# Optimization experiments

Hardware: AMD Instinct MI355X
Metric: run time of the kernel (lower is better)

The kernel has to match this reference:

```python
import jax, jax.numpy as jnp
import numpy as np

B, L, D, K = 32, 128, 400, 40
RTOL, ATOL = 1e-4, 1e-6


def setup_inputs() -> dict:
    key = jax.random.key(0)
    ks = jax.random.split(key, 9)
    s = 0.3                      # input scale keeps exp(energy) in fp32 range
    u = 1.0 / np.sqrt(D)         # param scale
    input_h = jax.random.normal(ks[0], (B, L, D), jnp.float32) * s
    input_c = jax.random.normal(ks[1], (B, L, D), jnp.float32) * s
    W_d = jax.random.normal(ks[2], (K, D), jnp.float32) * u
    W_e = jax.random.normal(ks[3], (K, D), jnp.float32) * u
    U = jax.random.normal(ks[4], (K, D, D), jnp.float32) * u
    b = jax.random.normal(ks[5], (K,), jnp.float32) * 0.1
    heads = jax.random.randint(ks[6], (B, L), 0, L)
    pos = jnp.arange(L)[None, :]
    heads = jnp.where(heads == pos, (heads + 1) % L, heads)  # no self-loops (diag is -inf)
    arc_tags = jax.random.randint(ks[7], (B, L), 0, K)
    lengths = jax.random.randint(ks[8], (B,), L // 2, L + 1)
    mask = (jnp.arange(L)[None, :] < lengths[:, None]).astype(jnp.float32)
    return {"input_h": input_h, "input_c": input_c, "W_d": W_d, "W_e": W_e,
            "U": U, "b": b, "mask": mask, "heads": heads,
            "arc_tags": arc_tags, "lengths": lengths}


def reference(input_h, input_c, W_d, W_e, U, b, mask, heads, arc_tags, lengths):
    Bsz, Ln, _ = input_h.shape
    # --- BiAAttention: energy[b,k,head,child] ---
    bil = jnp.einsum('bhd,kde,bce->bkhc', input_h, U, input_c)
    sd = jnp.einsum('kd,bhd->bkh', W_d, input_h)[:, :, :, None]   # head bias
    se = jnp.einsum('kd,bcd->bkc', W_e, input_c)[:, :, None, :]   # child bias
    energy = bil + sd + se + b[None, :, None, None]
    energy = energy * mask[:, None, :, None] * mask[:, None, None, :]
    eye = jnp.eye(Ln, dtype=energy.dtype)
    energy = energy + jnp.where(eye > 0, -jnp.inf, 0.0)           # no self-arcs
    # --- Matrix-Tree partition function ---
    A = jnp.exp(energy) * mask[:, None, :, None] * mask[:, None, None, :]
    A = A.sum(axis=1)                                             # [B,L,L] over labels
    Dg = A.sum(axis=1) * (1.0 + RTOL) + ATOL                      # column (in-degree) sums
    Lap = eye * Dg[:, None, :] - A                                # Laplacian
    Sub = Lap[:, 1:, 1:]                                          # drop root row/col
    valid = jnp.arange(Ln - 1)[None, :] < (lengths - 1)[:, None]
    vm = valid[:, :, None] & valid[:, None, :]
    Sub = jnp.where(vm, Sub, jnp.eye(Ln - 1, dtype=Sub.dtype))    # identity-pad = logdet of [1:len,1:len]
    z = jnp.linalg.slogdet(Sub)[1]                                # [B]
    # --- gold-tree energy ---
    bi = jnp.arange(Bsz)[:, None]
    pos = jnp.arange(Ln)[None, :]
    te = energy[bi, arc_tags, heads, pos]                         # [B,L]
    tgt = te[:, 1:].sum(axis=1)
    return z - tgt
```

## Files before the change

### kernel.cpp

```cpp
#include <hip/hip_runtime.h>
#include <hip/hip_bf16.h>

#define BB 32
#define LL 128
#define DD 400
#define KK 40
#define EE 416
#define SDN 50
#define SEN 52

typedef __attribute__((ext_vector_type(8)))  short  bfrag;
typedef __attribute__((ext_vector_type(16))) float  ffrag;

static __device__ __forceinline__ short f2bf(float f) {
    union { float f; unsigned u; } v; v.f = f;
    unsigned r = (v.u + 0x7FFF + ((v.u >> 16) & 1)) >> 16;
    return (short)r;
}

__global__ __launch_bounds__(256) void p_hc(
    const float* __restrict__ H, const float* __restrict__ C,
    short* __restrict__ Hs, short* __restrict__ Cs)
{
    int id = blockIdx.x * 256 + threadIdx.x;
    if (id < BB*SDN*LL) {
        int b = id / (SDN*LL); int r = id % (SDN*LL);
        int sd = r / LL; int h = r % LL;
        const float* src = H + ((size_t)(b*LL + h))*DD + sd*8;
        bfrag v;
#pragma unroll
        for (int j = 0; j < 8; ++j) v[j] = f2bf(src[j]);
        *(bfrag*)(Hs + (size_t)id*8) = v;
    } else {
        id -= BB*SDN*LL;
        int b = id / (SEN*LL); int r = id % (SEN*LL);
        int se = r / LL; int c = r % LL;
        bfrag v;
#pragma unroll
        for (int j = 0; j < 8; ++j) {
            int e = se*8 + j;
            v[j] = (e < DD) ? f2bf(C[((size_t)(b*LL + c))*DD + e]) : (short)0;
        }
        *(bfrag*)(Cs + (size_t)id*8) = v;
    }
}

__global__ __launch_bounds__(256) void p_u(
    const float* __restrict__ U, short* __restrict__ Us)
{
    int id = blockIdx.x * 256 + threadIdx.x;
    int k = id / (SDN*EE); int r = id % (SDN*EE);
    int sd = r / EE; int e = r % EE;
    bfrag v;
#pragma unroll
    for (int j = 0; j < 8; ++j)
        v[j] = (e < DD) ? f2bf(U[((size_t)k*DD + sd*8 + j)*DD + e]) : (short)0;
    *(bfrag*)(Us + (size_t)id*8) = v;
}

__global__ __launch_bounds__(256) void k_sdse(
    const float* __restrict__ H, const float* __restrict__ C,
    const float* __restrict__ Wd, const float* __restrict__ We,
    float* __restrict__ SD, float* __restrict__ SE)
{
    const int k = blockIdx.x % KK;
    const int b = blockIdx.x / KK;
    const int t = threadIdx.x;
    __shared__ float wd[DD], we[DD];
    for (int f = t; f < DD; f += 256) { wd[f] = Wd[k*DD + f]; we[f] = We[k*DD + f]; }
    __syncthreads();
    const int row = t & 127;
    const float* src = (t < 128) ? (H + (size_t)(b*LL + row)*DD)
                                 : (C + (size_t)(b*LL + row)*DD);
    const float* w = (t < 128) ? wd : we;
    float s = 0.f;
    for (int d = 0; d < DD; d += 4) {
        float4 v = *(const float4*)(src + d);
        s = fmaf(v.x, w[d+0], s); s = fmaf(v.y, w[d+1], s);
        s = fmaf(v.z, w[d+2], s); s = fmaf(v.w, w[d+3], s);
    }
    if (t < 128) SD[(b*KK + k)*LL + row] = s;
    else         SE[(b*KK + k)*LL + row] = s;
}

__global__ __launch_bounds__(256, 2) void k_mfma(
    const short* __restrict__ Hs, const short* __restrict__ Cs,
    const short* __restrict__ Us,
    const float* __restrict__ SD, const float* __restrict__ SE,
    const float* __restrict__ bvec, const float* __restrict__ mask,
    const int* __restrict__ heads, const int* __restrict__ tags,
    float* __restrict__ A8, float* __restrict__ tgt)
{
    const int k = blockIdx.x;
    const int b = blockIdx.y;
    const int t = threadIdx.x;
    const int w  = t >> 6;
    const int l  = t & 63;
    const int l31 = l & 31;
    const int kh  = l >> 5;
    const int wm  = w >> 1;
    const int wn  = w & 1;

    __shared__ short Tbuf[16*LL*8];

    ffrag Sacc[2][2];
#pragma unroll
    for (int a = 0; a < 2; ++a)
#pragma unroll
        for (int c2 = 0; c2 < 2; ++c2)
#pragma unroll
            for (int r = 0; r < 16; ++r) Sacc[a][c2][r] = 0.f;

    const size_t usK = (size_t)k * SDN * EE;
    const size_t hsB = (size_t)b * SDN * LL;
    const size_t csB = (size_t)b * SEN * LL;

    for (int chunk = 0; chunk < 4; ++chunk) {
        const int e0  = chunk * 128;
        const int NEc = (chunk < 3) ? 128 : 32;
        const int nmt = (NEc == 128) ? 2 : ((wm == 0) ? 1 : 0);

        ffrag Tacc[2][2];
#pragma unroll
        for (int a = 0; a < 2; ++a)
#pragma unroll
            for (int c2 = 0; c2 < 2; ++c2)
#pragma unroll
                for (int r = 0; r < 16; ++r) Tacc[a][c2][r] = 0.f;

        if (nmt > 0) {
            for (int ds = 0; ds < 25; ++ds) {
                const int sdl = 2*ds + kh;
                bfrag afr[2], bfr[2];
#pragma unroll
                for (int mt = 0; mt < 2; ++mt) {
                    if (mt < nmt) {
                        int eg = e0 + 64*wm + 32*mt + l31;
                        afr[mt] = *(const bfrag*)(Us + (usK + (size_t)sdl*EE + eg)*8);
                    }
                }
#pragma unroll
                for (int nt = 0; nt < 2; ++nt) {
                    int h = 64*wn + 32*nt + l31;
                    bfr[nt] = *(const bfrag*)(Hs + (hsB + (size_t)sdl*LL + h)*8);
                }
#pragma unroll
                for (int mt = 0; mt < 2; ++mt) {
                    if (mt < nmt) {
#pragma unroll
                        for (int nt = 0; nt < 2; ++nt)
                            Tacc[mt][nt] = __builtin_amdgcn_mfma_f32_32x32x16_bf16(
                                afr[mt], bfr[nt], Tacc[mt][nt], 0, 0, 0);
                    }
                }
            }
#pragma unroll
            for (int mt = 0; mt < 2; ++mt) {
                if (mt < nmt) {
#pragma unroll
                    for (int nt = 0; nt < 2; ++nt) {
                        int h = 64*wn + 32*nt + l31;
#pragma unroll
                        for (int r = 0; r < 16; r += 2) {
                            int e_loc = 64*wm + 32*mt + (r&3) + 8*(r>>2) + 4*kh;
                            int s_e = e_loc >> 3, e7 = e_loc & 7;
                            unsigned lo = (unsigned short)f2bf(Tacc[mt][nt][r]);
                            unsigned hi = (unsigned short)f2bf(Tacc[mt][nt][r+1]);
                            *(unsigned*)(&Tbuf[((size_t)s_e*LL + h)*8 + e7]) =
                                lo | (hi << 16);
                        }
                    }
                }
            }
        }
        __syncthreads();

        const int esteps = NEc >> 4;
        for (int es = 0; es < esteps; ++es) {
            const int sel = 2*es + kh;
            bfrag afr[2], bfr[2];
#pragma unroll
            for (int at = 0; at < 2; ++at) {
                int h = 64*wm + 32*at + l31;
                afr[at] = *(const bfrag*)(&Tbuf[((size_t)sel*LL + h)*8]);
            }
#pragma unroll
            for (int bt = 0; bt < 2; ++bt) {
                int c = 64*wn + 32*bt + l31;
                int seg = (e0 >> 3) + sel;
                bfr[bt] = *(const bfrag*)(Cs + (csB + (size_t)seg*LL + c)*8);
            }
#pragma unroll
            for (int at = 0; at < 2; ++at)
#pragma unroll
                for (int bt = 0; bt < 2; ++bt)
                    Sacc[at][bt] = __builtin_amdgcn_mfma_f32_32x32x16_bf16(
                        afr[at], bfr[bt], Sacc[at][bt], 0, 0, 0);
        }
        __syncthreads();
    }

    const float bk = bvec[k];
    const float* SDb = SD + ((size_t)b*KK + k)*LL;
    const float* SEb = SE + ((size_t)b*KK + k)*LL;
    float* Ab = A8 + ((size_t)((k & 7)*BB + b))*LL*LL;

#pragma unroll
    for (int at = 0; at < 2; ++at) {
#pragma unroll
        for (int bt = 0; bt < 2; ++bt) {
            const int c = 64*wn + 32*bt + l31;
            const float mc = mask[b*LL + c];
            const float sev = SEb[c];
            const int headc = heads[b*LL + c];
            const int tagc  = tags[b*LL + c];
#pragma unroll
            for (int r = 0; r < 16; ++r) {
                int h = 64*wm + 32*at + (r&3) + 8*(r>>2) + 4*kh;
                if (h == c) continue;
                float mh = mask[b*LL + h];
                if (mh == 0.f || mc == 0.f) continue;
                float eng = Sacc[at][bt][r] + SDb[h] + sev + bk;
                atomicAdd(&Ab[h*LL + c], __expf(eng));
                if (c >= 1 && tagc == k && headc == h) atomicAdd(&tgt[b], eng);
            }
        }
    }
}

__global__ __launch_bounds__(256) void k_logdet(
    const float* __restrict__ A8, const int* __restrict__ lengths,
    const float* __restrict__ tgt, float* __restrict__ out)
{
    const int b = blockIdx.x;
    const int t = threadIdx.x;
    const int rg = t >> 4;
    const int cg = t & 15;

    __shared__ float As[LL*LL];
    __shared__ float Dg[128];
    __shared__ float Lbuf[128];
    __shared__ float Ubuf[128];
    __shared__ float red[256];

    const float4* A4 = (const float4*)A8;
    for (int f4 = t; f4 < 4096; f4 += 256) {
        float4 s = make_float4(0.f, 0.f, 0.f, 0.f);
#pragma unroll
        for (int g = 0; g < 8; ++g) {
            float4 v = A4[((size_t)(g*BB + b))*4096 + f4];
            s.x += v.x; s.y += v.y; s.z += v.z; s.w += v.w;
        }
        ((float4*)As)[f4] = s;
    }
    __syncthreads();

    if (t < 128) {
        float s = 0.f;
        for (int hr = 0; hr < LL; ++hr) s += As[hr*LL + t];
        Dg[t] = s * (1.0f + 1e-4f) + 1e-6f;
    }
    __syncthreads();

    const int n1 = lengths[b] - 1;
    float m[8][8];
#pragma unroll
    for (int r = 0; r < 8; ++r) {
        const int i = 8*rg + r;
#pragma unroll
        for (int c = 0; c < 8; ++c) {
            const int j = 8*cg + c;
            float v;
            if (i < n1 && j < n1)
                v = ((i == j) ? Dg[i+1] : 0.f) - As[(i+1)*LL + (j+1)];
            else
                v = (i == j) ? 1.f : 0.f;
            m[r][c] = v;
        }
    }
    __syncthreads();

    for (int j = 0; j < 127; ++j) {
        const int jg = j >> 3, jl = j & 7;
        if (cg == jg) {
#pragma unroll
            for (int c = 0; c < 8; ++c) {
                if (c == jl) {
#pragma unroll
                    for (int r = 0; r < 8; ++r) Lbuf[8*rg + r] = m[r][c];
                }
            }
        }
        if (rg == jg) {
#pragma unroll
            for (int r = 0; r < 8; ++r) {
                if (r == jl) {
#pragma unroll
                    for (int c = 0; c < 8; ++c) Ubuf[8*cg + c] = m[r][c];
                }
            }
        }
        __syncthreads();

        const float piv = Lbuf[j];
        if (t == j) Dg[j] = piv;
        const float rp = 1.0f / piv;
        float lr[8], ur[8];
#pragma unroll
        for (int r = 0; r < 8; ++r) lr[r] = Lbuf[8*rg + r] * rp;
#pragma unroll
        for (int c = 0; c < 8; ++c) ur[c] = Ubuf[8*cg + c];
#pragma unroll
        for (int r = 0; r < 8; ++r)
#pragma unroll
            for (int c = 0; c < 8; ++c)
                m[r][c] = fmaf(-lr[r], ur[c], m[r][c]);
        __syncthreads();
    }

    float lsum = 0.f;
    if (t < 127) lsum = logf(Dg[t]);
    red[t] = lsum;
    __syncthreads();
    for (int off = 128; off >= 1; off >>= 1) {
        if (t < off) red[t] += red[t + off];
        __syncthreads();
    }
    if (t == 0) out[b] = red[0] - tgt[b];
}

extern "C" void kernel_launch(void* const* d_in, const int* in_sizes, int n_in,
                              void* d_out, int out_size, void* d_ws, size_t ws_size,
                              hipStream_t stream) {
    const float* H    = (const float*)d_in[0];
    const float* C    = (const float*)d_in[1];
    const float* Wd   = (const float*)d_in[2];
    const float* We   = (const float*)d_in[3];
    const float* U    = (const float*)d_in[4];
    const float* bv   = (const float*)d_in[5];
    const float* mask = (const float*)d_in[6];
    const int* heads  = (const int*)d_in[7];
    const int* tags   = (const int*)d_in[8];
    const int* lens   = (const int*)d_in[9];
    float* out = (float*)d_out;

    char* p = (char*)d_ws;
    float* A8  = (float*)p;                 p += (size_t)8*BB*LL*LL*4;
    float* tgt = (float*)p;                 p += 32*4;
    float* SDp = (float*)p;                 p += (size_t)BB*KK*LL*4;
    float* SEp = (float*)p;                 p += (size_t)BB*KK*LL*4;
    short* Hsp = (short*)p;                 p += (size_t)BB*SDN*LL*8*2;
    short* Csp = (short*)p;                 p += (size_t)BB*SEN*LL*8*2;
    short* Usp = (short*)p;                 p += (size_t)KK*SDN*EE*8*2;

    hipMemsetAsync(d_ws, 0, ((size_t)8*BB*LL*LL + 32)*4, stream);

    p_hc  <<<dim3(1632), 256, 0, stream>>>(H, C, Hsp, Csp);
    p_u   <<<dim3(3250), 256, 0, stream>>>(U, Usp);
    k_sdse<<<dim3(BB*KK), 256, 0, stream>>>(H, C, Wd, We, SDp, SEp);
    k_mfma<<<dim3(KK, BB), 256, 0, stream>>>(Hsp, Csp, Usp, SDp, SEp, bv, mask,
                                             heads, tags, A8, tgt);
    k_logdet<<<dim3(BB), 256, 0, stream>>>(A8, lens, tgt, out);
}
```

Measured before the change: 413.7 us.

## Merge prep kernels, prefetch MFMA operands, split A8 reduction into parallel kernel

Merges the three preprocessing kernels (H/C bf16 packing, U packing, SD/SE bias dots) into one launch with block-range dispatch, which removes two launch gaps. The MFMA kernel is restructured to loop over M-tiles with software-prefetched register operands for the next step, uses 32-bit indexing, and raises the occupancy hint to 3 blocks per CU. The 8-way partial-sum reduction of A8 moves out of the 32-block logdet kernel into a separate 512-block kernel. That spreads the bandwidth-heavy reduction across the whole GPU, at the cost of an extra launch and a round trip through an intermediate buffer.

```diff
diff --git a/kernel.cpp b/kernel.cpp
--- a/kernel.cpp
+++ b/kernel.cpp
@@ -18,72 +18,71 @@
     return (short)r;
 }
 
-__global__ __launch_bounds__(256) void p_hc(
+__global__ __launch_bounds__(256) void k_prep(
     const float* __restrict__ H, const float* __restrict__ C,
-    short* __restrict__ Hs, short* __restrict__ Cs)
-{
-    int id = blockIdx.x * 256 + threadIdx.x;
-    if (id < BB*SDN*LL) {
-        int b = id / (SDN*LL); int r = id % (SDN*LL);
-        int sd = r / LL; int h = r % LL;
-        const float* src = H + ((size_t)(b*LL + h))*DD + sd*8;
-        bfrag v;
-#pragma unroll
-        for (int j = 0; j < 8; ++j) v[j] = f2bf(src[j]);
-        *(bfrag*)(Hs + (size_t)id*8) = v;
-    } else {
-        id -= BB*SDN*LL;
-        int b = id / (SEN*LL); int r = id % (SEN*LL);
-        int se = r / LL; int c = r % LL;
-        bfrag v;
-#pragma unroll
-        for (int j = 0; j < 8; ++j) {
-            int e = se*8 + j;
-            v[j] = (e < DD) ? f2bf(C[((size_t)(b*LL + c))*DD + e]) : (short)0;
-        }
-        *(bfrag*)(Cs + (size_t)id*8) = v;
-    }
-}
-
-__global__ __launch_bounds__(256) void p_u(
-    const float* __restrict__ U, short* __restrict__ Us)
-{
-    int id = blockIdx.x * 256 + threadIdx.x;
-    int k = id / (SDN*EE); int r = id % (SDN*EE);
-    int sd = r / EE; int e = r % EE;
-    bfrag v;
-#pragma unroll
-    for (int j = 0; j < 8; ++j)
-        v[j] = (e < DD) ? f2bf(U[((size_t)k*DD + sd*8 + j)*DD + e]) : (short)0;
-    *(bfrag*)(Us + (size_t)id*8) = v;
-}
-
-__global__ __launch_bounds__(256) void k_sdse(
-    const float* __restrict__ H, const float* __restrict__ C,
+    const float* __restrict__ U,
     const float* __restrict__ Wd, const float* __restrict__ We,
+    short* __restrict__ Hs, short* __restrict__ Cs, short* __restrict__ Us,
     float* __restrict__ SD, float* __restrict__ SE)
 {
-    const int k = blockIdx.x % KK;
-    const int b = blockIdx.x / KK;
+    const int bid = blockIdx.x;
     const int t = threadIdx.x;
-    __shared__ float wd[DD], we[DD];
-    for (int f = t; f < DD; f += 256) { wd[f] = Wd[k*DD + f]; we[f] = We[k*DD + f]; }
-    __syncthreads();
-    const int row = t & 127;
-    const float* src = (t < 128) ? (H + (size_t)(b*LL + row)*DD)
-                                 : (C + (size_t)(b*LL + row)*DD);
-    const float* w = (t < 128) ? wd : we;
-    float s = 0.f;
-    for (int d = 0; d < DD; d += 4) {
-        float4 v = *(const float4*)(src + d);
-        s = fmaf(v.x, w[d+0], s); s = fmaf(v.y, w[d+1], s);
-        s = fmaf(v.z, w[d+2], s); s = fmaf(v.w, w[d+3], s);
-    }
-    if (t < 128) SD[(b*KK + k)*LL + row] = s;
-    else         SE[(b*KK + k)*LL + row] = s;
-}
-
-__global__ __launch_bounds__(256, 2) void k_mfma(
+    __shared__ float wsh[2*DD];
+
+    if (bid < 1632) {
+        int id = bid * 256 + t;
+        if (id < BB*SDN*LL) {
+            int b = id / (SDN*LL); int r = id % (SDN*LL);
+            int sd = r / LL; int h = r % LL;
+            const float* src = H + ((size_t)(b*LL + h))*DD + sd*8;
+            bfrag v;
+#pragma unroll
+            for (int j = 0; j < 8; ++j) v[j] = f2bf(src[j]);
+            *(bfrag*)(Hs + (size_t)id*8) = v;
+        } else {
+            id -= BB*SDN*LL;
+            int b = id / (SEN*LL); int r = id % (SEN*LL);
+            int se = r / LL; int c = r % LL;
+            bfrag v;
+#pragma unroll
+            for (int j = 0; j < 8; ++j) {
+                int e = se*8 + j;
+                v[j] = (e < DD) ? f2bf(C[((size_t)(b*LL + c))*DD + e]) : (short)0;
+            }
+            *(bfrag*)(Cs + (size_t)id*8) = v;
+        }
+    } else if (bid < 4882) {
+        int id = (bid - 1632) * 256 + t;
+        int k = id / (SDN*EE); int r = id % (SDN*EE);
+        int sd = r / EE; int e = r % EE;
+        bfrag v;
+#pragma unroll
+        for (int j = 0; j < 8; ++j)
+            v[j] = (e < DD) ? f2bf(U[((size_t)k*DD + sd*8 + j)*DD + e]) : (short)0;
+        *(bfrag*)(Us + (size_t)id*8) = v;
+    } else {
+        int sb = bid - 4882;
+        const int k = sb % KK;
+        const int b = sb / KK;
+        float* wd = wsh; float* we = wsh + DD;
+        for (int f = t; f < DD; f += 256) { wd[f] = Wd[k*DD + f]; we[f] = We[k*DD + f]; }
+        __syncthreads();
+        const int row = t & 127;
+        const float* src = (t < 128) ? (H + (size_t)(b*LL + row)*DD)
+                                     : (C + (size_t)(b*LL + row)*DD);
+        const float* w = (t < 128) ? wd : we;
+        float s = 0.f;
+        for (int d = 0; d < DD; d += 4) {
+            float4 v = *(const float4*)(src + d);
+            s = fmaf(v.x, w[d+0], s); s = fmaf(v.y, w[d+1], s);
+            s = fmaf(v.z, w[d+2], s); s = fmaf(v.w, w[d+3], s);
+        }
+        if (t < 128) SD[(b*KK + k)*LL + row] = s;
+        else         SE[(b*KK + k)*LL + row] = s;
+    }
+}
+
+__global__ __launch_bounds__(256, 3) void k_mfma(
     const short* __restrict__ Hs, const short* __restrict__ Cs,
     const short* __restrict__ Us,
     const float* __restrict__ SD, const float* __restrict__ SE,
@@ -103,6 +102,10 @@
 
     __shared__ short Tbuf[16*LL*8];
 
+    const bfrag* UsF = (const bfrag*)Us;
+    const bfrag* HsF = (const bfrag*)Hs;
+    const bfrag* CsF = (const bfrag*)Cs;
+
     ffrag Sacc[2][2];
 #pragma unroll
     for (int a = 0; a < 2; ++a)
@@ -111,91 +114,73 @@
 #pragma unroll
             for (int r = 0; r < 16; ++r) Sacc[a][c2][r] = 0.f;
 
-    const size_t usK = (size_t)k * SDN * EE;
-    const size_t hsB = (size_t)b * SDN * LL;
-    const size_t csB = (size_t)b * SEN * LL;
+    const int usK = k * (SDN * EE);
+    const int hsB = b * (SDN * LL);
+    const int csB = b * (SEN * LL);
 
     for (int chunk = 0; chunk < 4; ++chunk) {
         const int e0  = chunk * 128;
         const int NEc = (chunk < 3) ? 128 : 32;
         const int nmt = (NEc == 128) ? 2 : ((wm == 0) ? 1 : 0);
 
-        ffrag Tacc[2][2];
-#pragma unroll
-        for (int a = 0; a < 2; ++a)
-#pragma unroll
-            for (int c2 = 0; c2 < 2; ++c2)
-#pragma unroll
-                for (int r = 0; r < 16; ++r) Tacc[a][c2][r] = 0.f;
-
-        if (nmt > 0) {
+        for (int mt = 0; mt < nmt; ++mt) {
+            ffrag T0, T1;
+#pragma unroll
+            for (int r = 0; r < 16; ++r) { T0[r] = 0.f; T1[r] = 0.f; }
+            const int eg = e0 + 64*wm + 32*mt + l31;
+            const int hg = 64*wn + l31;
+            bfrag aC  = UsF[usK + kh*EE + eg];
+            bfrag b0C = HsF[hsB + kh*LL + hg];
+            bfrag b1C = HsF[hsB + kh*LL + hg + 32];
             for (int ds = 0; ds < 25; ++ds) {
-                const int sdl = 2*ds + kh;
-                bfrag afr[2], bfr[2];
-#pragma unroll
-                for (int mt = 0; mt < 2; ++mt) {
-                    if (mt < nmt) {
-                        int eg = e0 + 64*wm + 32*mt + l31;
-                        afr[mt] = *(const bfrag*)(Us + (usK + (size_t)sdl*EE + eg)*8);
-                    }
+                bfrag aN = aC, b0N = b0C, b1N = b1C;
+                if (ds < 24) {
+                    const int sdl = 2*ds + 2 + kh;
+                    aN  = UsF[usK + sdl*EE + eg];
+                    b0N = HsF[hsB + sdl*LL + hg];
+                    b1N = HsF[hsB + sdl*LL + hg + 32];
                 }
-#pragma unroll
-                for (int nt = 0; nt < 2; ++nt) {
-                    int h = 64*wn + 32*nt + l31;
-                    bfr[nt] = *(const bfrag*)(Hs + (hsB + (size_t)sdl*LL + h)*8);
+                T0 = __builtin_amdgcn_mfma_f32_32x32x16_bf16(aC, b0C, T0, 0, 0, 0);
+                T1 = __builtin_amdgcn_mfma_f32_32x32x16_bf16(aC, b1C, T1, 0, 0, 0);
+                aC = aN; b0C = b0N; b1C = b1N;
+            }
+#pragma unroll
+            for (int nt = 0; nt < 2; ++nt) {
+                const int h = 64*wn + 32*nt + l31;
+#pragma unroll
+                for (int r = 0; r < 16; r += 2) {
+                    int e_loc = 64*wm + 32*mt + (r&3) + 8*(r>>2) + 4*kh;
+                    int s_e = e_loc >> 3, e7 = e_loc & 7;
+                    float v0 = nt ? T1[r]   : T0[r];
+                    float v1 = nt ? T1[r+1] : T0[r+1];
+                    unsigned lo = (unsigned short)f2bf(v0);
+                    unsigned hi = (unsigned short)f2bf(v1);
+                    *(unsigned*)(&Tbuf[((size_t)s_e*LL + h)*8 + e7]) = lo | (hi << 16);
                 }
-#pragma unroll
-                for (int mt = 0; mt < 2; ++mt) {
-                    if (mt < nmt) {
-#pragma unroll
-                        for (int nt = 0; nt < 2; ++nt)
-                            Tacc[mt][nt] = __builtin_amdgcn_mfma_f32_32x32x16_bf16(
-                                afr[mt], bfr[nt], Tacc[mt][nt], 0, 0, 0);
-                    }
-                }
-            }
-#pragma unroll
-            for (int mt = 0; mt < 2; ++mt) {
-                if (mt < nmt) {
-#pragma unroll
-                    for (int nt = 0; nt < 2; ++nt) {
-                        int h = 64*wn + 32*nt + l31;
-#pragma unroll
-                        for (int r = 0; r < 16; r += 2) {
-                            int e_loc = 64*wm + 32*mt + (r&3) + 8*(r>>2) + 4*kh;
-                            int s_e = e_loc >> 3, e7 = e_loc & 7;
-                            unsigned lo = (unsigned short)f2bf(Tacc[mt][nt][r]);
-                            unsigned hi = (unsigned short)f2bf(Tacc[mt][nt][r+1]);
-                            *(unsigned*)(&Tbuf[((size_t)s_e*LL + h)*8 + e7]) =
-                                lo | (hi << 16);
-                        }
-                    }
-                }
             }
         }
         __syncthreads();
 
         const int esteps = NEc >> 4;
+        const int cg0 = 64*wn + l31;
+        const int hgA = 64*wm + l31;
+        const int segBase = e0 >> 3;
+        bfrag c0C = CsF[csB + (segBase + kh)*LL + cg0];
+        bfrag c1C = CsF[csB + (segBase + kh)*LL + cg0 + 32];
         for (int es = 0; es < esteps; ++es) {
             const int sel = 2*es + kh;
-            bfrag afr[2], bfr[2];
-#pragma unroll
-            for (int at = 0; at < 2; ++at) {
-                int h = 64*wm + 32*at + l31;
-                afr[at] = *(const bfrag*)(&Tbuf[((size_t)sel*LL + h)*8]);
-            }
-#pragma unroll
-            for (int bt = 0; bt < 2; ++bt) {
-                int c = 64*wn + 32*bt + l31;
-                int seg = (e0 >> 3) + sel;
-                bfr[bt] = *(const bfrag*)(Cs + (csB + (size_t)seg*LL + c)*8);
-            }
-#pragma unroll
-            for (int at = 0; at < 2; ++at)
-#pragma unroll
-                for (int bt = 0; bt < 2; ++bt)
-                    Sacc[at][bt] = __builtin_amdgcn_mfma_f32_32x32x16_bf16(
-                        afr[at], bfr[bt], Sacc[at][bt], 0, 0, 0);
+            bfrag c0N = c0C, c1N = c1C;
+            if (es + 1 < esteps) {
+                c0N = CsF[csB + (segBase + sel + 2)*LL + cg0];
+                c1N = CsF[csB + (segBase + sel + 2)*LL + cg0 + 32];
+            }
+            bfrag a0 = *(const bfrag*)(&Tbuf[((size_t)sel*LL + hgA)*8]);
+            bfrag a1 = *(const bfrag*)(&Tbuf[((size_t)sel*LL + hgA + 32)*8]);
+            Sacc[0][0] = __builtin_amdgcn_mfma_f32_32x32x16_bf16(a0, c0C, Sacc[0][0], 0, 0, 0);
+            Sacc[0][1] = __builtin_amdgcn_mfma_f32_32x32x16_bf16(a0, c1C, Sacc[0][1], 0, 0, 0);
+            Sacc[1][0] = __builtin_amdgcn_mfma_f32_32x32x16_bf16(a1, c0C, Sacc[1][0], 0, 0, 0);
+            Sacc[1][1] = __builtin_amdgcn_mfma_f32_32x32x16_bf16(a1, c1C, Sacc[1][1], 0, 0, 0);
+            c0C = c0N; c1C = c1N;
         }
         __syncthreads();
     }
@@ -228,8 +213,22 @@
     }
 }
 
+__global__ __launch_bounds__(256) void k_asum(
+    const float4* __restrict__ A8, float4* __restrict__ As)
+{
+    const int f4 = blockIdx.x * 256 + threadIdx.x;
+    const int b = f4 >> 12, r = f4 & 4095;
+    float4 s = make_float4(0.f, 0.f, 0.f, 0.f);
+#pragma unroll
+    for (int g = 0; g < 8; ++g) {
+        float4 v = A8[((size_t)(g*BB + b))*4096 + r];
+        s.x += v.x; s.y += v.y; s.z += v.z; s.w += v.w;
+    }
+    As[f4] = s;
+}
+
 __global__ __launch_bounds__(256) void k_logdet(
-    const float* __restrict__ A8, const int* __restrict__ lengths,
+    const float* __restrict__ Asg, const int* __restrict__ lengths,
     const float* __restrict__ tgt, float* __restrict__ out)
 {
     const int b = blockIdx.x;
@@ -243,16 +242,9 @@
     __shared__ float Ubuf[128];
     __shared__ float red[256];
 
-    const float4* A4 = (const float4*)A8;
-    for (int f4 = t; f4 < 4096; f4 += 256) {
-        float4 s = make_float4(0.f, 0.f, 0.f, 0.f);
-#pragma unroll
-        for (int g = 0; g < 8; ++g) {
-            float4 v = A4[((size_t)(g*BB + b))*4096 + f4];
-            s.x += v.x; s.y += v.y; s.z += v.z; s.w += v.w;
-        }
-        ((float4*)As)[f4] = s;
-    }
+    const float4* As4 = (const float4*)Asg;
+    for (int f4 = t; f4 < 4096; f4 += 256)
+        ((float4*)As)[f4] = As4[(size_t)b*4096 + f4];
     __syncthreads();
 
     if (t < 128) {
@@ -347,6 +339,7 @@
     char* p = (char*)d_ws;
     float* A8  = (float*)p;                 p += (size_t)8*BB*LL*LL*4;
     float* tgt = (float*)p;                 p += 32*4;
+    float* As  = (float*)p;                 p += (size_t)BB*LL*LL*4;
     float* SDp = (float*)p;                 p += (size_t)BB*KK*LL*4;
     float* SEp = (float*)p;                 p += (size_t)BB*KK*LL*4;
     short* Hsp = (short*)p;                 p += (size_t)BB*SDN*LL*8*2;
@@ -355,10 +348,9 @@
 
     hipMemsetAsync(d_ws, 0, ((size_t)8*BB*LL*LL + 32)*4, stream);
 
-    p_hc  <<<dim3(1632), 256, 0, stream>>>(H, C, Hsp, Csp);
-    p_u   <<<dim3(3250), 256, 0, stream>>>(U, Usp);
-    k_sdse<<<dim3(BB*KK), 256, 0, stream>>>(H, C, Wd, We, SDp, SEp);
+    k_prep<<<dim3(6162), 256, 0, stream>>>(H, C, U, Wd, We, Hsp, Csp, Usp, SDp, SEp);
     k_mfma<<<dim3(KK, BB), 256, 0, stream>>>(Hsp, Csp, Usp, SDp, SEp, bv, mask,
                                              heads, tags, A8, tgt);
-    k_logdet<<<dim3(BB), 256, 0, stream>>>(A8, lens, tgt, out);
-}
+    k_asum<<<dim3(512), 256, 0, stream>>>((const float4*)A8, (float4*)As);
+    k_logdet<<<dim3(BB), 256, 0, stream>>>(As, lens, tgt, out);
+}
```

Measured after the change: 868.0 us. +109.8%, slower.
